# Kernel tuning notes

Hardware: AMD Instinct MI355X
Metric: run time of the kernel (lower is better)

## Reference

```python
import jax, jax.numpy as jnp
import numpy as np

BETA = 0.25
N_E = 1024
E_DIM = 64


def setup_inputs() -> dict:
    key = jax.random.key(0)
    k1, k2 = jax.random.split(key)
    z = jax.random.normal(k1, (32, E_DIM, 64, 64), dtype=jnp.float32)  # (B,C,H,W)
    emb = jax.random.uniform(k2, (N_E, E_DIM), dtype=jnp.float32,
                             minval=-1.0 / N_E, maxval=1.0 / N_E)
    return {"z": z, "embedding": emb}


def reference(z, embedding):
    # (B,C,H,W) -> (B,H,W,C)
    z_nhwc = jnp.transpose(z, (0, 2, 3, 1))
    zf = z_nhwc.reshape(-1, E_DIM)  # (N, C)
    # squared L2 distances: ||z||^2 + ||e||^2 - 2 z e^T  -> (N, n_e)
    d = (jnp.sum(zf * zf, axis=1, keepdims=True)
         + jnp.sum(embedding * embedding, axis=1)
         - 2.0 * jnp.matmul(zf, embedding.T))
    min_encoding_indices = jnp.argmin(d, axis=1)[:, None]  # (N,1)
    idx = min_encoding_indices[:, 0]
    min_encodings = jax.nn.one_hot(idx, N_E, dtype=jnp.float32)  # (N, n_e)
    # codebook lookup (equivalent to one-hot matmul)
    z_q = embedding[idx].reshape(z_nhwc.shape)  # (B,H,W,C)
    loss = (jnp.mean((jax.lax.stop_gradient(z_q) - z_nhwc) ** 2)
            + BETA * jnp.mean((z_q - jax.lax.stop_gradient(z_nhwc)) ** 2))
    # straight-through estimator
    z_q = z_nhwc + jax.lax.stop_gradient(z_q - z_nhwc)
    e_mean = jnp.mean(min_encodings, axis=0)
    perplexity = jnp.exp(-jnp.sum(e_mean * jnp.log(e_mean + 1e-10)))
    z_q = jnp.transpose(z_q, (0, 3, 1, 2))  # (B,C,H,W)
    return (loss, z_q, perplexity, min_encodings, min_encoding_indices)
```

## Files before the change

### kernel.cpp

```cpp
#include <hip/hip_runtime.h>

#define N_PIX   (32 * 64 * 64)
#define E_DIM   64
#define N_E     1024
#define Z_ELEMS (N_PIX * E_DIM)

#define LOSS_OFF 0
#define ZQ_OFF   1
#define PERP_OFF (1 + Z_ELEMS)
#define ENC_OFF  ((size_t)(2 + Z_ELEMS))
#define IDX_OFF  (ENC_OFF + (size_t)N_PIX * N_E)

#define WS_COUNTS   0
#define WS_LOSS     4096
#define WS_EE       8192
#define WS_EMB16    12288
#define WS_KEYS     143360
#define WS_CAND     1191936
#define WS_WCOUNT   5386240
#define NWAVES      4096
#define WAVE_CAP    256
#define MARGIN      4e-3f

typedef float f32x2 __attribute__((ext_vector_type(2)));
typedef float f32x4 __attribute__((ext_vector_type(4)));
typedef short bf16x8 __attribute__((ext_vector_type(8)));
typedef unsigned long long u64;
typedef unsigned short ushort;

__device__ __forceinline__ float dpp_add_xor1(float v) {
    int i = __builtin_bit_cast(int, v);
    i = __builtin_amdgcn_mov_dpp(i, 0xB1, 0xF, 0xF, true);
    return v + __builtin_bit_cast(float, i);
}
__device__ __forceinline__ float dpp_add_xor2(float v) {
    int i = __builtin_bit_cast(int, v);
    i = __builtin_amdgcn_mov_dpp(i, 0x4E, 0xF, 0xF, true);
    return v + __builtin_bit_cast(float, i);
}
__device__ __forceinline__ ushort rne_bf16(float f) {
    unsigned u = __builtin_bit_cast(unsigned, f);
    return (ushort)((u + 0x7FFFu + ((u >> 16) & 1u)) >> 16);
}

__device__ __forceinline__ void zero_row(float* rowb, int tid) {
    if (tid < 255) {
        const f32x4 z4 = {0.f, 0.f, 0.f, 0.f};
        __builtin_nontemporal_store(z4, (f32x4*)(rowb + 2 + 4 * tid));
    } else {
        const f32x2 z2 = {0.f, 0.f};
        __builtin_nontemporal_store(z2, (f32x2*)rowb);
        __builtin_nontemporal_store(z2, (f32x2*)(rowb + 1022));
    }
}

__global__ void vq_prep(const float* __restrict__ emb, float* __restrict__ ee,
                        ushort* __restrict__ emb16) {
    int e = blockIdx.x * blockDim.x + threadIdx.x;
    if (e < N_E) {
        const float* r = emb + e * E_DIM;
        float s0 = 0.f, s1 = 0.f, s2 = 0.f, s3 = 0.f;
        #pragma unroll
        for (int c = 0; c < E_DIM; c += 4) {
            s0 = fmaf(r[c],     r[c],     s0);
            s1 = fmaf(r[c + 1], r[c + 1], s1);
            s2 = fmaf(r[c + 2], r[c + 2], s2);
            s3 = fmaf(r[c + 3], r[c + 3], s3);
        }
        ee[e] = (s0 + s1) + (s2 + s3);
        #pragma unroll
        for (int j = 0; j < 64; j += 8) {
            bf16x8 v;
            #pragma unroll
            for (int q = 0; q < 8; ++q) v[q] = (short)rne_bf16(r[j + q]);
            *(bf16x8*)(emb16 + e * E_DIM + j) = v;
        }
    }
}

__device__ __forceinline__ bf16x8 load_afrag(const float* __restrict__ z,
                                             int px16, int lane, int khalf) {
    const int px = px16 + (lane & 15);
    const int b  = px >> 12;
    const int hw = px & 4095;
    const int c0 = khalf * 32 + ((lane >> 4) << 3);
    const float* zp = z + ((size_t)(b * E_DIM + c0)) * 4096 + hw;
    bf16x8 v;
    #pragma unroll
    for (int j = 0; j < 8; ++j) v[j] = (short)rne_bf16(zp[(size_t)j * 4096]);
    return v;
}

__global__ __launch_bounds__(256, 4) void vq_scan(
    const float* __restrict__ z, const ushort* __restrict__ emb16,
    const float* __restrict__ ee, float* __restrict__ out,
    unsigned* __restrict__ cand, unsigned* __restrict__ wcount)
{
    const int tid  = threadIdx.x;
    const int lane = tid & 63;
    const int pxb  = blockIdx.x * 128 + (tid >> 6) * 32;

    bf16x8 afr[2][2];
    #pragma unroll
    for (int t = 0; t < 2; ++t)
        #pragma unroll
        for (int h = 0; h < 2; ++h)
            afr[t][h] = load_afrag(z, pxb + t * 16, lane, h);

    float m[2][4];
    #pragma unroll
    for (int t = 0; t < 2; ++t)
        #pragma unroll
        for (int r = 0; r < 4; ++r) m[t][r] = 3.4e38f;

    const size_t zb = ENC_OFF + (size_t)blockIdx.x * 128 * N_E;
    const int col = lane & 15;
    const int bko = ((lane >> 4) << 3);

    for (int cg = 0; cg < 64; ++cg) {
        const float eev = ee[cg * 16 + col];
        const ushort* br = emb16 + (cg * 16 + col) * E_DIM + bko;
        const bf16x8 b0 = *(const bf16x8*)br;
        const bf16x8 b1 = *(const bf16x8*)(br + 32);
        #pragma unroll
        for (int t = 0; t < 2; ++t) {
            f32x4 acc = {0.f, 0.f, 0.f, 0.f};
            acc = __builtin_amdgcn_mfma_f32_16x16x32_bf16(afr[t][0], b0, acc, 0, 0, 0);
            acc = __builtin_amdgcn_mfma_f32_16x16x32_bf16(afr[t][1], b1, acc, 0, 0, 0);
            #pragma unroll
            for (int r = 0; r < 4; ++r)
                m[t][r] = fminf(m[t][r], fmaf(-2.f, acc[r], eev));
        }
        zero_row(out + zb + (size_t)cg * N_E, tid);
    }

    float lim[2][4];
    #pragma unroll
    for (int t = 0; t < 2; ++t)
        #pragma unroll
        for (int r = 0; r < 4; ++r) {
            float v = m[t][r];
            v = fminf(v, __shfl_xor(v, 1));
            v = fminf(v, __shfl_xor(v, 2));
            v = fminf(v, __shfl_xor(v, 4));
            v = fminf(v, __shfl_xor(v, 8));
            lim[t][r] = v + MARGIN;
        }

    const unsigned wid  = blockIdx.x * 4 + (tid >> 6);
    unsigned* wseg = cand + (size_t)wid * WAVE_CAP;
    const u64 below = (lane == 0) ? 0ull : ((~0ull) >> (64 - lane));
    unsigned wbase = 0;

    for (int cg = 0; cg < 64; ++cg) {
        const float eev = ee[cg * 16 + col];
        const ushort* br = emb16 + (cg * 16 + col) * E_DIM + bko;
        const bf16x8 b0 = *(const bf16x8*)br;
        const bf16x8 b1 = *(const bf16x8*)(br + 32);
        #pragma unroll
        for (int t = 0; t < 2; ++t) {
            f32x4 acc = {0.f, 0.f, 0.f, 0.f};
            acc = __builtin_amdgcn_mfma_f32_16x16x32_bf16(afr[t][0], b0, acc, 0, 0, 0);
            acc = __builtin_amdgcn_mfma_f32_16x16x32_bf16(afr[t][1], b1, acc, 0, 0, 0);
            #pragma unroll
            for (int r = 0; r < 4; ++r) {
                const float d = fmaf(-2.f, acc[r], eev);
                const bool hit = (d <= lim[t][r]);
                const u64 mask = __ballot(hit);
                if (hit) {
                    const unsigned pos = wbase + (unsigned)__popcll(mask & below);
                    if (pos < WAVE_CAP) {
                        const unsigned px = pxb + t * 16 + ((lane >> 4) << 2) + r;
                        wseg[pos] = (px << 10) | (unsigned)(cg * 16 + col);
                    }
                }
                wbase += (unsigned)__popcll(mask);
            }
        }
        zero_row(out + zb + (size_t)(64 + cg) * N_E, tid);
    }

    if (lane == 0) wcount[wid] = (wbase < WAVE_CAP) ? wbase : WAVE_CAP;
}

__global__ __launch_bounds__(256) void vq_cleanup(
    const float* __restrict__ z, const float* __restrict__ emb,
    const float* __restrict__ ee, const unsigned* __restrict__ cand,
    const unsigned* __restrict__ wcount, u64* __restrict__ keys)
{
    const int s = threadIdx.x & 3;
    const unsigned quad = threadIdx.x >> 2;
    const unsigned w = blockIdx.x;
    const unsigned n = wcount[w];

    for (unsigned j = quad; j < n; j += 64) {
        const unsigned ent = cand[(size_t)w * WAVE_CAP + j];
        const int p = ent >> 10, k = ent & 1023;
        const int b = p >> 12, hw = p & 4095;

        const float* zp = z + ((size_t)(b * E_DIM + s * 16)) * 4096 + hw;
        f32x4 zv[4];
        #pragma unroll
        for (int m = 0; m < 4; ++m)
            #pragma unroll
            for (int qi = 0; qi < 4; ++qi)
                zv[m][qi] = zp[(size_t)(4 * m + qi) * 4096];

        f32x4 za = {0.f,0.f,0.f,0.f};
        #pragma unroll
        for (int j2 = 0; j2 < 4; ++j2) za = __builtin_elementwise_fma(zv[j2], zv[j2], za);
        f32x2 zt = __builtin_shufflevector(za, za, 0, 1)
                 + __builtin_shufflevector(za, za, 2, 3);
        const float zz = dpp_add_xor2(dpp_add_xor1(zt.x + zt.y));

        const f32x4* rp = (const f32x4*)(emb + k * E_DIM) + s * 4;
        f32x4 a = {0.f,0.f,0.f,0.f};
        #pragma unroll
        for (int j2 = 0; j2 < 4; ++j2) a = __builtin_elementwise_fma(zv[j2], rp[j2], a);
        f32x2 t2 = __builtin_shufflevector(a, a, 0, 1)
                 + __builtin_shufflevector(a, a, 2, 3);
        const float dot = dpp_add_xor2(dpp_add_xor1(t2.x + t2.y));
        const float d = zz + ee[k] - 2.0f * dot;

        if (s == 0) {
            const u64 key = ((u64)__builtin_bit_cast(unsigned, d) << 32) | (unsigned)k;
            atomicMin(&keys[p], key);
        }
    }
}

__global__ __launch_bounds__(256) void vq_resolve(
    const float* __restrict__ z, const float* __restrict__ emb,
    const u64* __restrict__ keys, float* __restrict__ out,
    unsigned* __restrict__ counts, double* __restrict__ loss_acc)
{
    const int p  = blockIdx.x * 256 + threadIdx.x;
    const int b  = p >> 12;
    const int hw = p & 4095;
    const int idx = (int)(unsigned)(keys[p] & 0xFFFFFFFFu);

    out[IDX_OFF + p] = (float)idx;
    out[ENC_OFF + (size_t)p * N_E + idx] = 1.0f;
    atomicAdd(&counts[idx], 1u);

    const f32x4* eb = (const f32x4*)(emb + idx * E_DIM);
    const float* zp = z + (size_t)b * E_DIM * 4096 + hw;
    float* zqp = out + ZQ_OFF + (size_t)b * E_DIM * 4096 + hw;
    f32x4 la = {0.f,0.f,0.f,0.f};
    #pragma unroll
    for (int m = 0; m < 16; ++m) {
        const f32x4 q = eb[m];
        f32x4 zq4;
        #pragma unroll
        for (int qi = 0; qi < 4; ++qi) {
            zq4[qi] = zp[(size_t)(4 * m + qi) * 4096];
            __builtin_nontemporal_store(q[qi], &zqp[(size_t)(4 * m + qi) * 4096]);
        }
        const f32x4 dq = q - zq4;
        la = __builtin_elementwise_fma(dq, dq, la);
    }
    float lsum = (la[0] + la[2]) + (la[1] + la[3]);
    #pragma unroll
    for (int o = 32; o > 0; o >>= 1) lsum += __shfl_down(lsum, o);
    if ((threadIdx.x & 63) == 0) atomicAdd(loss_acc, (double)lsum);
}

__global__ void vq_final(const unsigned* __restrict__ counts,
                         const double* __restrict__ loss_acc,
                         float* __restrict__ out)
{
    __shared__ float red[N_E];
    const int e = threadIdx.x;
    const float em = (float)counts[e] * (1.0f / (float)N_PIX);
    red[e] = em * logf(em + 1e-10f);
    __syncthreads();
    for (int s = 512; s > 0; s >>= 1) {
        if (e < s) red[e] += red[e + s];
        __syncthreads();
    }
    if (e == 0) {
        out[PERP_OFF] = expf(-red[0]);
        out[LOSS_OFF] = (float)((*loss_acc) * (1.25 / (double)Z_ELEMS));
    }
}

extern "C" void kernel_launch(void* const* d_in, const int* in_sizes, int n_in,
                              void* d_out, int out_size, void* d_ws, size_t ws_size,
                              hipStream_t stream) {
    const float* z   = (const float*)d_in[0];
    const float* emb = (const float*)d_in[1];
    float* out = (float*)d_out;
    char* ws = (char*)d_ws;

    unsigned* counts   = (unsigned*)(ws + WS_COUNTS);
    double*   loss_acc = (double*)(ws + WS_LOSS);
    float*    ee       = (float*)(ws + WS_EE);
    ushort*   emb16    = (ushort*)(ws + WS_EMB16);
    u64*      keys     = (u64*)(ws + WS_KEYS);
    unsigned* cand     = (unsigned*)(ws + WS_CAND);
    unsigned* wcount   = (unsigned*)(ws + WS_WCOUNT);

    (void)hipMemsetAsync(ws, 0, 4104, stream);
    (void)hipMemsetAsync(keys, 0xFF, (size_t)N_PIX * 8, stream);
    vq_prep<<<4, 256, 0, stream>>>(emb, ee, emb16);
    vq_scan<<<N_PIX / 128, 256, 0, stream>>>(z, emb16, ee, out, cand, wcount);
    vq_cleanup<<<NWAVES, 256, 0, stream>>>(z, emb, ee, cand, wcount, keys);
    vq_resolve<<<N_PIX / 256, 256, 0, stream>>>(z, emb, keys, out, counts, loss_acc);
    vq_final<<<1, N_E, 0, stream>>>(counts, loss_acc, out);
}
```

Before: 267.9 us.

## Fuse candidate cleanup and resolve into one kernel with shared-memory argmin keys

Merges the cleanup and resolve kernels so each block handles one wave's 32 pixels, computing the argmin in shared memory instead of global 64-bit atomics on a keys array. It also removes both memsets by zeroing counts and the loss accumulator in the prep kernel. The intent is to save two memset launches, one kernel launch and the global key traffic. The cost is that only 32 threads per block do the z_q and loss write-back, which may lower memory-level parallelism in that phase.

```diff
diff --git a/kernel.cpp b/kernel.cpp
--- a/kernel.cpp
+++ b/kernel.cpp
@@ -15,9 +15,8 @@
 #define WS_LOSS     4096
 #define WS_EE       8192
 #define WS_EMB16    12288
-#define WS_KEYS     143360
-#define WS_CAND     1191936
-#define WS_WCOUNT   5386240
+#define WS_CAND     143360
+#define WS_WCOUNT   4337664
 #define NWAVES      4096
 #define WAVE_CAP    256
 #define MARGIN      4e-3f
@@ -55,9 +54,12 @@
 }
 
 __global__ void vq_prep(const float* __restrict__ emb, float* __restrict__ ee,
-                        ushort* __restrict__ emb16) {
+                        ushort* __restrict__ emb16, unsigned* __restrict__ counts,
+                        double* __restrict__ loss_acc) {
     int e = blockIdx.x * blockDim.x + threadIdx.x;
     if (e < N_E) {
+        counts[e] = 0u;
+        if (e == 0) *loss_acc = 0.0;
         const float* r = emb + e * E_DIM;
         float s0 = 0.f, s1 = 0.f, s2 = 0.f, s3 = 0.f;
         #pragma unroll
@@ -183,18 +185,27 @@
     if (lane == 0) wcount[wid] = (wbase < WAVE_CAP) ? wbase : WAVE_CAP;
 }
 
-__global__ __launch_bounds__(256) void vq_cleanup(
+__global__ __launch_bounds__(256, 4) void vq_finish(
     const float* __restrict__ z, const float* __restrict__ emb,
     const float* __restrict__ ee, const unsigned* __restrict__ cand,
-    const unsigned* __restrict__ wcount, u64* __restrict__ keys)
+    const unsigned* __restrict__ wcount, float* __restrict__ out,
+    unsigned* __restrict__ counts, double* __restrict__ loss_acc)
 {
-    const int s = threadIdx.x & 3;
-    const unsigned quad = threadIdx.x >> 2;
+    __shared__ u64 lkey[32];
+
     const unsigned w = blockIdx.x;
+    const int pxb = (int)(w * 32);
+    const int tid = threadIdx.x;
+    const int s = tid & 3;
+    const unsigned quad = tid >> 2;
+
+    if (tid < 32) lkey[tid] = ~0ull;
+    __syncthreads();
+
     const unsigned n = wcount[w];
-
+    const unsigned* seg = cand + (size_t)w * WAVE_CAP;
     for (unsigned j = quad; j < n; j += 64) {
-        const unsigned ent = cand[(size_t)w * WAVE_CAP + j];
+        const unsigned ent = seg[j];
         const int p = ent >> 10, k = ent & 1023;
         const int b = p >> 12, hw = p & 4095;
 
@@ -224,45 +235,42 @@
 
         if (s == 0) {
             const u64 key = ((u64)__builtin_bit_cast(unsigned, d) << 32) | (unsigned)k;
-            atomicMin(&keys[p], key);
-        }
-    }
-}
-
-__global__ __launch_bounds__(256) void vq_resolve(
-    const float* __restrict__ z, const float* __restrict__ emb,
-    const u64* __restrict__ keys, float* __restrict__ out,
-    unsigned* __restrict__ counts, double* __restrict__ loss_acc)
-{
-    const int p  = blockIdx.x * 256 + threadIdx.x;
-    const int b  = p >> 12;
-    const int hw = p & 4095;
-    const int idx = (int)(unsigned)(keys[p] & 0xFFFFFFFFu);
-
-    out[IDX_OFF + p] = (float)idx;
-    out[ENC_OFF + (size_t)p * N_E + idx] = 1.0f;
-    atomicAdd(&counts[idx], 1u);
-
-    const f32x4* eb = (const f32x4*)(emb + idx * E_DIM);
-    const float* zp = z + (size_t)b * E_DIM * 4096 + hw;
-    float* zqp = out + ZQ_OFF + (size_t)b * E_DIM * 4096 + hw;
-    f32x4 la = {0.f,0.f,0.f,0.f};
-    #pragma unroll
-    for (int m = 0; m < 16; ++m) {
-        const f32x4 q = eb[m];
-        f32x4 zq4;
-        #pragma unroll
-        for (int qi = 0; qi < 4; ++qi) {
-            zq4[qi] = zp[(size_t)(4 * m + qi) * 4096];
-            __builtin_nontemporal_store(q[qi], &zqp[(size_t)(4 * m + qi) * 4096]);
-        }
-        const f32x4 dq = q - zq4;
-        la = __builtin_elementwise_fma(dq, dq, la);
-    }
-    float lsum = (la[0] + la[2]) + (la[1] + la[3]);
-    #pragma unroll
-    for (int o = 32; o > 0; o >>= 1) lsum += __shfl_down(lsum, o);
-    if ((threadIdx.x & 63) == 0) atomicAdd(loss_acc, (double)lsum);
+            atomicMin(&lkey[p - pxb], key);
+        }
+    }
+    __syncthreads();
+
+    if (tid < 32) {
+        const int p  = pxb + tid;
+        const int b  = p >> 12;
+        const int hw = p & 4095;
+        const int idx = (int)(unsigned)(lkey[tid] & 0xFFFFFFFFu);
+
+        out[IDX_OFF + p] = (float)idx;
+        out[ENC_OFF + (size_t)p * N_E + idx] = 1.0f;
+        atomicAdd(&counts[idx], 1u);
+
+        const f32x4* eb = (const f32x4*)(emb + idx * E_DIM);
+        const float* zp = z + (size_t)b * E_DIM * 4096 + hw;
+        float* zqp = out + ZQ_OFF + (size_t)b * E_DIM * 4096 + hw;
+        f32x4 la = {0.f,0.f,0.f,0.f};
+        #pragma unroll
+        for (int m = 0; m < 16; ++m) {
+            const f32x4 q = eb[m];
+            f32x4 zq4;
+            #pragma unroll
+            for (int qi = 0; qi < 4; ++qi) {
+                zq4[qi] = zp[(size_t)(4 * m + qi) * 4096];
+                __builtin_nontemporal_store(q[qi], &zqp[(size_t)(4 * m + qi) * 4096]);
+            }
+            const f32x4 dq = q - zq4;
+            la = __builtin_elementwise_fma(dq, dq, la);
+        }
+        float lsum = (la[0] + la[2]) + (la[1] + la[3]);
+        #pragma unroll
+        for (int o = 16; o > 0; o >>= 1) lsum += __shfl_down(lsum, o);
+        if (tid == 0) atomicAdd(loss_acc, (double)lsum);
+    }
 }
 
 __global__ void vq_final(const unsigned* __restrict__ counts,
@@ -296,15 +304,12 @@
     double*   loss_acc = (double*)(ws + WS_LOSS);
     float*    ee       = (float*)(ws + WS_EE);
     ushort*   emb16    = (ushort*)(ws + WS_EMB16);
-    u64*      keys     = (u64*)(ws + WS_KEYS);
     unsigned* cand     = (unsigned*)(ws + WS_CAND);
     unsigned* wcount   = (unsigned*)(ws + WS_WCOUNT);
 
-    (void)hipMemsetAsync(ws, 0, 4104, stream);
-    (void)hipMemsetAsync(keys, 0xFF, (size_t)N_PIX * 8, stream);
-    vq_prep<<<4, 256, 0, stream>>>(emb, ee, emb16);
+    vq_prep<<<4, 256, 0, stream>>>(emb, ee, emb16, counts, loss_acc);
     vq_scan<<<N_PIX / 128, 256, 0, stream>>>(z, emb16, ee, out, cand, wcount);
-    vq_cleanup<<<NWAVES, 256, 0, stream>>>(z, emb, ee, cand, wcount, keys);
-    vq_resolve<<<N_PIX / 256, 256, 0, stream>>>(z, emb, keys, out, counts, loss_acc);
+    vq_finish<<<NWAVES, 256, 0, stream>>>(z, emb, ee, cand, wcount, out,
+                                          counts, loss_acc);
     vq_final<<<1, N_E, 0, stream>>>(counts, loss_acc, out);
 }
```

Result: faster. 248.0 us (-7.4%).
